# Kernel tuning notes

Measured on AMD Instinct MI355X. Metric: run time of the kernel, lower is better.

Reference implementation:

```python
import jax, jax.numpy as jnp
import numpy as np

N = 50000        # nodes
E = 800000       # edges (avg degree 16)
IN = 256         # in_size
H = 4            # heads
C = 32           # out_size per head
NEG_SLOPE = 0.2  # PyG GATConv leaky_relu slope
LN_EPS = 1e-5


def setup_inputs() -> dict:
    key = jax.random.key(0)
    ks = jax.random.split(key, 6)
    x = jax.random.normal(ks[0], (N, IN), dtype=jnp.float32)
    edge_index = jax.random.randint(ks[1], (2, E), 0, N, dtype=jnp.int32)
    W = jax.random.normal(ks[2], (IN, H * C), dtype=jnp.float32) * 0.05
    att_src = jax.random.normal(ks[3], (H, C), dtype=jnp.float32) * 0.05
    att_dst = jax.random.normal(ks[4], (H, C), dtype=jnp.float32) * 0.05
    bias = jnp.zeros((H * C,), dtype=jnp.float32)
    ln_gamma = jnp.ones((H * C,), dtype=jnp.float32)
    ln_beta = jnp.zeros((H * C,), dtype=jnp.float32)
    return {"x": x, "edge_index": edge_index, "W": W, "att_src": att_src,
            "att_dst": att_dst, "bias": bias, "ln_gamma": ln_gamma,
            "ln_beta": ln_beta}


def _segment_softmax(alpha, seg, num_segments):
    # alpha: [E, H], softmax over edges sharing the same destination node.
    amax = jax.ops.segment_max(alpha, seg, num_segments=num_segments)  # [N, H]
    amax = jnp.where(jnp.isfinite(amax), amax, 0.0)  # nodes with no in-edges
    ex = jnp.exp(alpha - amax[seg])
    denom = jax.ops.segment_sum(ex, seg, num_segments=num_segments)    # [N, H]
    return ex / (denom[seg] + 1e-16)


def reference(x, edge_index, W, att_src, att_dst, bias, ln_gamma, ln_beta):
    # --- GATConv (concat=True) ---
    x_lin = (x @ W).reshape(N, H, C)                    # [N, H, C]
    a_src = jnp.sum(x_lin * att_src, axis=-1)           # [N, H]
    a_dst = jnp.sum(x_lin * att_dst, axis=-1)           # [N, H]
    src, dst = edge_index[0], edge_index[1]             # messages src -> dst
    alpha = a_src[src] + a_dst[dst]                     # [E, H]
    alpha = jnp.where(alpha >= 0, alpha, NEG_SLOPE * alpha)
    alpha = _segment_softmax(alpha, dst, N)             # [E, H]
    msg = x_lin[src] * alpha[..., None]                 # [E, H, C]
    out = jax.ops.segment_sum(msg, dst, num_segments=N) # [N, H, C]
    out = out.reshape(N, H * C) + bias                  # [N, H*C]
    # --- LayerNorm over feature dim ---
    mu = jnp.mean(out, axis=-1, keepdims=True)
    var = jnp.mean(jnp.square(out - mu), axis=-1, keepdims=True)
    out = (out - mu) * jax.lax.rsqrt(var + LN_EPS) * ln_gamma + ln_beta
    # --- activation ---
    return jax.nn.relu(out)
```

## Files before the change

kernel.cpp:

```cpp
#include <hip/hip_runtime.h>

#define NNODES 50000
#define NEDGES 800000
#define INFEAT 256
#define HC 128
#define NH 4
#define CPH 32
#define LSTRIDE 264
#define CSTRIDE 16

typedef unsigned int uint32;
typedef unsigned short u16;
typedef short short8 __attribute__((ext_vector_type(8)));
typedef float f32x4 __attribute__((ext_vector_type(4)));

__device__ __forceinline__ float b2f(u16 s) {
    uint32 u = ((uint32)s) << 16;
    return __builtin_bit_cast(float, u);
}
__device__ __forceinline__ u16 f2bf(float x) {
    uint32 u = __builtin_bit_cast(uint32, x);
    uint32 r = (u + 0x7FFFu + ((u >> 16) & 1u)) >> 16;
    return (u16)r;
}
__device__ __forceinline__ bool probe_bf16(const void* gamma) {
    return ((const uint32*)gamma)[0] == 0x3F803F80u;
}

__global__ __launch_bounds__(256) void wtp_kernel(const void* __restrict__ W,
                                                  const void* __restrict__ gm,
                                                  u16* __restrict__ wtp,
                                                  int* __restrict__ count) {
    const bool isbf = probe_bf16(gm);
    int c = blockIdx.x * 256 + threadIdx.x;
    int kt = c >> 9, nt = (c >> 6) & 7, l = c & 63;
    int r = l & 15, quad = l >> 4;
    int n = nt * 16 + r;
    int kbase = kt * 32 + quad * 8;
    u16 vals[8];
#pragma unroll
    for (int j = 0; j < 8; ++j) {
        int k = kbase + j;
        vals[j] = isbf ? ((const u16*)W)[k * HC + n] : f2bf(((const float*)W)[k * HC + n]);
    }
    *(uint4*)(wtp + (size_t)c * 8) = *(const uint4*)vals;
    uint4 z = {0u, 0u, 0u, 0u};
    uint4* cz = (uint4*)count;
    for (int i = c; i < NNODES * CSTRIDE / 4; i += 4096) cz[i] = z;
}

__global__ __launch_bounds__(256) void hist_kernel(const int* __restrict__ ei,
                                                   int* __restrict__ count,
                                                   int* __restrict__ rank) {
    int eb = blockIdx.x * 1024 + threadIdx.x;
#pragma unroll
    for (int rep = 0; rep < 4; ++rep) {
        int e = eb + rep * 256;
        if (e < NEDGES) rank[e] = atomicAdd(&count[ei[NEDGES + e] * CSTRIDE], 1);
    }
}

__global__ __launch_bounds__(256) void gemm_mfma(const void* __restrict__ x,
                                                 const uint4* __restrict__ wtp,
                                                 const void* __restrict__ att_src,
                                                 const void* __restrict__ att_dst,
                                                 const void* __restrict__ gm,
                                                 u16* __restrict__ xlin,
                                                 float* __restrict__ asrc,
                                                 float* __restrict__ adst) {
    __shared__ u16 atile[4 * 16 * LSTRIDE];
    const bool isbf = probe_bf16(gm);
    const int tid = threadIdx.x;
    const int wv = tid >> 6;
    const int lane = tid & 63;
    int wave = blockIdx.x * 4 + wv;
    int r = lane & 15;
    int quad = lane >> 4;
    int m0 = wave * 16;
    u16* my = atile + wv * (16 * LSTRIDE);

    if (isbf) {
#pragma unroll
        for (int rep = 0; rep < 8; ++rep) {
            int idx = rep * 64 + lane;
            int row = idx >> 5;
            int ch  = idx & 31;
            int gr = m0 + row;
            if (gr > NNODES - 1) gr = NNODES - 1;
            uint4 q = *(const uint4*)((const u16*)x + (size_t)gr * INFEAT + ch * 8);
            *(uint4*)(my + row * LSTRIDE + ch * 8) = q;
        }
    } else {
#pragma unroll
        for (int rep = 0; rep < 16; ++rep) {
            int idx = rep * 64 + lane;
            int row = idx >> 6;
            int c4  = idx & 63;
            int gr = m0 + row;
            if (gr > NNODES - 1) gr = NNODES - 1;
            float4 f = *(const float4*)((const float*)x + (size_t)gr * INFEAT + c4 * 4);
            u16 v[4] = {f2bf(f.x), f2bf(f.y), f2bf(f.z), f2bf(f.w)};
            *(uint2*)(my + row * LSTRIDE + c4 * 4) = *(const uint2*)v;
        }
    }
    __syncthreads();

    f32x4 acc[8];
#pragma unroll
    for (int nt = 0; nt < 8; ++nt) acc[nt] = (f32x4){0.f, 0.f, 0.f, 0.f};

#pragma unroll
    for (int kt = 0; kt < 8; ++kt) {
        short8 afrag = __builtin_bit_cast(short8,
            *(const uint4*)(my + r * LSTRIDE + kt * 32 + quad * 8));
#pragma unroll
        for (int nt = 0; nt < 8; ++nt) {
            short8 bfrag = __builtin_bit_cast(short8, wtp[(kt * 8 + nt) * 64 + lane]);
            acc[nt] = __builtin_amdgcn_mfma_f32_16x16x32_bf16(afrag, bfrag, acc[nt], 0, 0, 0);
        }
    }
#pragma unroll
    for (int nt = 0; nt < 8; ++nt) {
#pragma unroll
        for (int reg = 0; reg < 4; ++reg) {
            int grow = m0 + quad * 4 + reg;
            if (grow < NNODES) xlin[(size_t)grow * HC + nt * 16 + r] = f2bf(acc[nt][reg]);
        }
    }

    float asv[8], adv[8];
#pragma unroll
    for (int nt = 0; nt < 8; ++nt) {
        int c = nt * 16 + r;
        if (isbf) {
            asv[nt] = b2f(((const u16*)att_src)[c]);
            adv[nt] = b2f(((const u16*)att_dst)[c]);
        } else {
            asv[nt] = ((const float*)att_src)[c];
            adv[nt] = ((const float*)att_dst)[c];
        }
    }
    float psrc[4][4], pdst[4][4];
#pragma unroll
    for (int h = 0; h < 4; ++h)
#pragma unroll
        for (int reg = 0; reg < 4; ++reg) { psrc[h][reg] = 0.f; pdst[h][reg] = 0.f; }
#pragma unroll
    for (int nt = 0; nt < 8; ++nt) {
        const int h = nt >> 1;
#pragma unroll
        for (int reg = 0; reg < 4; ++reg) {
            psrc[h][reg] = fmaf(acc[nt][reg], asv[nt], psrc[h][reg]);
            pdst[h][reg] = fmaf(acc[nt][reg], adv[nt], pdst[h][reg]);
        }
    }
#pragma unroll
    for (int m = 1; m < 16; m <<= 1) {
#pragma unroll
        for (int h = 0; h < 4; ++h)
#pragma unroll
            for (int reg = 0; reg < 4; ++reg) {
                psrc[h][reg] += __shfl_xor(psrc[h][reg], m);
                pdst[h][reg] += __shfl_xor(pdst[h][reg], m);
            }
    }
#pragma unroll
    for (int reg = 0; reg < 4; ++reg)
#pragma unroll
        for (int h = 0; h < 4; ++h)
            if (r == reg * 4 + h) {
                int grow = m0 + quad * 4 + reg;
                if (grow < NNODES) {
                    asrc[grow * 4 + h] = psrc[h][reg];
                    adst[grow * 4 + h] = pdst[h][reg];
                }
            }
}

__global__ __launch_bounds__(256) void blkred_kernel(const int* __restrict__ count,
                                                     int* __restrict__ blksum) {
    int i = blockIdx.x * 256 + threadIdx.x;
    int v = (i < NNODES) ? count[i * CSTRIDE] : 0;
#pragma unroll
    for (int m = 1; m < 64; m <<= 1) v += __shfl_xor(v, m);
    __shared__ int s[4];
    if ((threadIdx.x & 63) == 0) s[threadIdx.x >> 6] = v;
    __syncthreads();
    if (threadIdx.x == 0) blksum[blockIdx.x] = s[0] + s[1] + s[2] + s[3];
}

__global__ __launch_bounds__(256) void scanout_kernel(const int* __restrict__ count,
                                                      const int* __restrict__ blksum,
                                                      int* __restrict__ offsets) {
    __shared__ int sb[256];
    __shared__ int sd[256];
    const int nblk = (NNODES + 255) / 256;
    int t = threadIdx.x;
    int bv = (t < nblk) ? blksum[t] : 0;
    sb[t] = bv;
    __syncthreads();
    for (int off = 1; off < 256; off <<= 1) {
        int tv = (t >= off) ? sb[t - off] : 0;
        __syncthreads();
        sb[t] += tv;
        __syncthreads();
    }
    int base = sb[blockIdx.x] - blksum[blockIdx.x];

    int i = blockIdx.x * 256 + t;
    int v = (i < NNODES) ? count[i * CSTRIDE] : 0;
    sd[t] = v;
    __syncthreads();
    for (int off = 1; off < 256; off <<= 1) {
        int tv = (t >= off) ? sd[t - off] : 0;
        __syncthreads();
        sd[t] += tv;
        __syncthreads();
    }
    if (i < NNODES) offsets[i] = base + sd[t] - v;
    if (i == 0) offsets[NNODES] = NEDGES;
}

__global__ __launch_bounds__(256) void scatter_kernel(const int* __restrict__ ei,
                                                      const int* __restrict__ offsets,
                                                      const int* __restrict__ rank,
                                                      int* __restrict__ col) {
    int e = blockIdx.x * 256 + threadIdx.x;
    if (e >= NEDGES) return;
    int d = ei[NEDGES + e];
    col[offsets[d] + rank[e]] = ei[e];
}

__global__ __launch_bounds__(256) void node_kernel(const u16* __restrict__ xlin,
                                                   const float* __restrict__ asrc,
                                                   const float* __restrict__ adst,
                                                   const int* __restrict__ offsets,
                                                   const int* __restrict__ col,
                                                   const void* __restrict__ bias,
                                                   const void* __restrict__ gamma,
                                                   const void* __restrict__ beta,
                                                   void* __restrict__ out) {
    const bool isbf = probe_bf16(gamma);
    int node = blockIdx.x * 4 + (threadIdx.x >> 6);
    int lane = threadIdx.x & 63;
    int h = lane >> 4;
    int f2 = lane * 2;
    float adh = adst[node * 4 + h];
    int start = offsets[node];
    int end = offsets[node + 1];

    float dsum = 0.f, acc0 = 0.f, acc1 = 0.f;
    int i = start;
    for (; i + 7 < end; i += 8) {
        int cc[8];
        uint32 pf[8];
        float aw[8];
#pragma unroll
        for (int j = 0; j < 8; ++j) cc[j] = col[i + j];
#pragma unroll
        for (int j = 0; j < 8; ++j) {
            pf[j] = *(const uint32*)(xlin + (size_t)cc[j] * HC + f2);
            aw[j] = asrc[cc[j] * 4 + h];
        }
#pragma unroll
        for (int j = 0; j < 8; ++j) {
            float a = aw[j] + adh;
            a = (a >= 0.f) ? a : 0.2f * a;
            float w = __expf(a);
            dsum += w;
            float x0 = __builtin_bit_cast(float, pf[j] << 16);
            float x1 = __builtin_bit_cast(float, pf[j] & 0xffff0000u);
            acc0 = fmaf(x0, w, acc0);
            acc1 = fmaf(x1, w, acc1);
        }
    }
    for (; i + 3 < end; i += 4) {
        int cc[4];
        uint32 pf[4];
        float aw[4];
#pragma unroll
        for (int j = 0; j < 4; ++j) cc[j] = col[i + j];
#pragma unroll
        for (int j = 0; j < 4; ++j) {
            pf[j] = *(const uint32*)(xlin + (size_t)cc[j] * HC + f2);
            aw[j] = asrc[cc[j] * 4 + h];
        }
#pragma unroll
        for (int j = 0; j < 4; ++j) {
            float a = aw[j] + adh;
            a = (a >= 0.f) ? a : 0.2f * a;
            float w = __expf(a);
            dsum += w;
            float x0 = __builtin_bit_cast(float, pf[j] << 16);
            float x1 = __builtin_bit_cast(float, pf[j] & 0xffff0000u);
            acc0 = fmaf(x0, w, acc0);
            acc1 = fmaf(x1, w, acc1);
        }
    }
    for (; i < end; ++i) {
        int c = col[i];
        uint32 p = *(const uint32*)(xlin + (size_t)c * HC + f2);
        float a = asrc[c * 4 + h] + adh;
        a = (a >= 0.f) ? a : 0.2f * a;
        float w = __expf(a);
        dsum += w;
        float x0 = __builtin_bit_cast(float, p << 16);
        float x1 = __builtin_bit_cast(float, p & 0xffff0000u);
        acc0 = fmaf(x0, w, acc0);
        acc1 = fmaf(x1, w, acc1);
    }
    float rden = 1.f / (dsum + 1e-16f);

    float bi0, bi1, g0, g1, be0, be1;
    if (isbf) {
        uint32 bb = ((const uint32*)bias)[lane];
        uint32 gg = ((const uint32*)gamma)[lane];
        uint32 eb = ((const uint32*)beta)[lane];
        bi0 = b2f((u16)(bb & 0xffffu)); bi1 = b2f((u16)(bb >> 16));
        g0  = b2f((u16)(gg & 0xffffu)); g1  = b2f((u16)(gg >> 16));
        be0 = b2f((u16)(eb & 0xffffu)); be1 = b2f((u16)(eb >> 16));
    } else {
        float2 tb = ((const float2*)bias)[lane];
        float2 tg = ((const float2*)gamma)[lane];
        float2 te = ((const float2*)beta)[lane];
        bi0 = tb.x; bi1 = tb.y; g0 = tg.x; g1 = tg.y; be0 = te.x; be1 = te.y;
    }
    float v0 = fmaf(acc0, rden, bi0);
    float v1 = fmaf(acc1, rden, bi1);
    float s2 = v0 + v1;
    float q2 = v0 * v0 + v1 * v1;
#pragma unroll
    for (int m = 1; m < 64; m <<= 1) {
        s2 += __shfl_xor(s2, m);
        q2 += __shfl_xor(q2, m);
    }
    float mean = s2 * (1.f / 128.f);
    float var = q2 * (1.f / 128.f) - mean * mean;
    float inv = rsqrtf(var + 1e-5f);
    float d0 = v0 - mean, d1 = v1 - mean;
    float o0 = fmaxf(fmaf(d0 * inv, g0, be0), 0.f);
    float o1 = fmaxf(fmaf(d1 * inv, g1, be1), 0.f);
    if (isbf) {
        uint32 po = (uint32)f2bf(o0) | ((uint32)f2bf(o1) << 16);
        ((uint32*)out)[(size_t)node * 64 + lane] = po;
    } else {
        float2 po; po.x = o0; po.y = o1;
        ((float2*)out)[(size_t)node * 64 + lane] = po;
    }
}

extern "C" void kernel_launch(void* const* d_in, const int* in_sizes, int n_in,
                              void* d_out, int out_size, void* d_ws, size_t ws_size,
                              hipStream_t stream) {
    const void* x       = d_in[0];
    const int*  ei      = (const int*)d_in[1];
    const void* W       = d_in[2];
    const void* att_src = d_in[3];
    const void* att_dst = d_in[4];
    const void* bias    = d_in[5];
    const void* gamma   = d_in[6];
    const void* beta    = d_in[7];

    char* w = (char*)d_ws;
    size_t off = 0;
    u16* xlin    = (u16*)(w + off);   off += 12800000;
    u16* wtp     = (u16*)(w + off);   off += 65536;
    float* asrc  = (float*)(w + off); off += 800000;
    float* adst  = (float*)(w + off); off += 800000;
    int* count   = (int*)(w + off);
    int* col     = (int*)(w + off);   off += 3200000;
    int* offsets = (int*)(w + off);   off += 200016;
    int* rank    = (int*)(w + off);   off += 3200000;
    int* blksum  = (int*)(w + off);   off += 1024;

    const int NBLK = (NNODES + 255) / 256;
    wtp_kernel<<<16, 256, 0, stream>>>(W, gamma, wtp, count);
    hist_kernel<<<(NEDGES + 1023) / 1024, 256, 0, stream>>>(ei, count, rank);
    gemm_mfma<<<(NNODES + 63) / 64, 256, 0, stream>>>(x, (const uint4*)wtp, att_src, att_dst,
                                                      gamma, xlin, asrc, adst);
    blkred_kernel<<<NBLK, 256, 0, stream>>>(count, blksum);
    scanout_kernel<<<NBLK, 256, 0, stream>>>(count, blksum, offsets);
    scatter_kernel<<<(NEDGES + 255) / 256, 256, 0, stream>>>(ei, offsets, rank, col);
    node_kernel<<<NNODES / 4, 256, 0, stream>>>(xlin, asrc, adst, offsets, col,
                                                bias, gamma, beta, d_out);
}
```

Measured before the change: 213.8 us.

## Precompute edge attention weights in CSR order during scatter; densify count array

The scatter kernel now computes the leaky-relu/exp attention weight for all four heads of every edge and writes them in CSR slot order. The node kernel then streams these weights instead of gathering asrc per neighbor and recomputing exp. The count array drops its 16-int padding, and the barrier after the wave-private LDS fill in the GEMM is removed. In exchange it adds a 12.8 MB write and read of per-edge weights, and packs the atomics onto shared cache lines. The new path only runs if the workspace is large enough.

Result: slower. 231.4 us (+8.2%).

```diff
diff --git a/kernel.cpp b/kernel.cpp
--- a/kernel.cpp
+++ b/kernel.cpp
@@ -7,7 +7,6 @@
 #define NH 4
 #define CPH 32
 #define LSTRIDE 264
-#define CSTRIDE 16
 
 typedef unsigned int uint32;
 typedef unsigned short u16;
@@ -46,7 +45,7 @@
     *(uint4*)(wtp + (size_t)c * 8) = *(const uint4*)vals;
     uint4 z = {0u, 0u, 0u, 0u};
     uint4* cz = (uint4*)count;
-    for (int i = c; i < NNODES * CSTRIDE / 4; i += 4096) cz[i] = z;
+    for (int i = c; i < NNODES / 4; i += 4096) cz[i] = z;
 }
 
 __global__ __launch_bounds__(256) void hist_kernel(const int* __restrict__ ei,
@@ -56,7 +55,7 @@
 #pragma unroll
     for (int rep = 0; rep < 4; ++rep) {
         int e = eb + rep * 256;
-        if (e < NEDGES) rank[e] = atomicAdd(&count[ei[NEDGES + e] * CSTRIDE], 1);
+        if (e < NEDGES) rank[e] = atomicAdd(&count[ei[NEDGES + e]], 1);
     }
 }
 
@@ -103,7 +102,6 @@
             *(uint2*)(my + row * LSTRIDE + c4 * 4) = *(const uint2*)v;
         }
     }
-    __syncthreads();
 
     f32x4 acc[8];
 #pragma unroll
@@ -180,7 +178,7 @@
 __global__ __launch_bounds__(256) void blkred_kernel(const int* __restrict__ count,
                                                      int* __restrict__ blksum) {
     int i = blockIdx.x * 256 + threadIdx.x;
-    int v = (i < NNODES) ? count[i * CSTRIDE] : 0;
+    int v = (i < NNODES) ? count[i] : 0;
 #pragma unroll
     for (int m = 1; m < 64; m <<= 1) v += __shfl_xor(v, m);
     __shared__ int s[4];
@@ -208,7 +206,7 @@
     int base = sb[blockIdx.x] - blksum[blockIdx.x];
 
     int i = blockIdx.x * 256 + t;
-    int v = (i < NNODES) ? count[i * CSTRIDE] : 0;
+    int v = (i < NNODES) ? count[i] : 0;
     sd[t] = v;
     __syncthreads();
     for (int off = 1; off < 256; off <<= 1) {
@@ -221,21 +219,39 @@
     if (i == 0) offsets[NNODES] = NEDGES;
 }
 
+template <bool WITHW>
 __global__ __launch_bounds__(256) void scatter_kernel(const int* __restrict__ ei,
                                                       const int* __restrict__ offsets,
                                                       const int* __restrict__ rank,
-                                                      int* __restrict__ col) {
+                                                      const float* __restrict__ asrc,
+                                                      const float* __restrict__ adst,
+                                                      int* __restrict__ col,
+                                                      float* __restrict__ wf) {
     int e = blockIdx.x * 256 + threadIdx.x;
     if (e >= NEDGES) return;
+    int s = ei[e];
     int d = ei[NEDGES + e];
-    col[offsets[d] + rank[e]] = ei[e];
-}
-
+    int slot = offsets[d] + rank[e];
+    col[slot] = s;
+    if (WITHW) {
+        float4 as = *(const float4*)(asrc + (size_t)s * 4);
+        float4 ad = *(const float4*)(adst + (size_t)d * 4);
+        float4 w;
+        float a0 = as.x + ad.x; a0 = (a0 >= 0.f) ? a0 : 0.2f * a0; w.x = __expf(a0);
+        float a1 = as.y + ad.y; a1 = (a1 >= 0.f) ? a1 : 0.2f * a1; w.y = __expf(a1);
+        float a2 = as.z + ad.z; a2 = (a2 >= 0.f) ? a2 : 0.2f * a2; w.z = __expf(a2);
+        float a3 = as.w + ad.w; a3 = (a3 >= 0.f) ? a3 : 0.2f * a3; w.w = __expf(a3);
+        *(float4*)(wf + (size_t)slot * 4) = w;
+    }
+}
+
+template <bool WITHW>
 __global__ __launch_bounds__(256) void node_kernel(const u16* __restrict__ xlin,
                                                    const float* __restrict__ asrc,
                                                    const float* __restrict__ adst,
                                                    const int* __restrict__ offsets,
                                                    const int* __restrict__ col,
+                                                   const float* __restrict__ wf,
                                                    const void* __restrict__ bias,
                                                    const void* __restrict__ gamma,
                                                    const void* __restrict__ beta,
@@ -245,69 +261,124 @@
     int lane = threadIdx.x & 63;
     int h = lane >> 4;
     int f2 = lane * 2;
-    float adh = adst[node * 4 + h];
+    float adh = WITHW ? 0.f : adst[node * 4 + h];
     int start = offsets[node];
     int end = offsets[node + 1];
 
     float dsum = 0.f, acc0 = 0.f, acc1 = 0.f;
     int i = start;
-    for (; i + 7 < end; i += 8) {
-        int cc[8];
-        uint32 pf[8];
-        float aw[8];
-#pragma unroll
-        for (int j = 0; j < 8; ++j) cc[j] = col[i + j];
-#pragma unroll
-        for (int j = 0; j < 8; ++j) {
-            pf[j] = *(const uint32*)(xlin + (size_t)cc[j] * HC + f2);
-            aw[j] = asrc[cc[j] * 4 + h];
-        }
-#pragma unroll
-        for (int j = 0; j < 8; ++j) {
-            float a = aw[j] + adh;
+    if (WITHW) {
+        for (; i + 7 < end; i += 8) {
+            int cc[8];
+            uint32 pf[8];
+            float wv[8];
+#pragma unroll
+            for (int j = 0; j < 8; ++j) cc[j] = col[i + j];
+#pragma unroll
+            for (int j = 0; j < 8; ++j) {
+                pf[j] = *(const uint32*)(xlin + (size_t)cc[j] * HC + f2);
+                wv[j] = wf[(size_t)(i + j) * 4 + h];
+            }
+#pragma unroll
+            for (int j = 0; j < 8; ++j) {
+                float w = wv[j];
+                dsum += w;
+                float x0 = __builtin_bit_cast(float, pf[j] << 16);
+                float x1 = __builtin_bit_cast(float, pf[j] & 0xffff0000u);
+                acc0 = fmaf(x0, w, acc0);
+                acc1 = fmaf(x1, w, acc1);
+            }
+        }
+        for (; i + 3 < end; i += 4) {
+            int cc[4];
+            uint32 pf[4];
+            float wv[4];
+#pragma unroll
+            for (int j = 0; j < 4; ++j) cc[j] = col[i + j];
+#pragma unroll
+            for (int j = 0; j < 4; ++j) {
+                pf[j] = *(const uint32*)(xlin + (size_t)cc[j] * HC + f2);
+                wv[j] = wf[(size_t)(i + j) * 4 + h];
+            }
+#pragma unroll
+            for (int j = 0; j < 4; ++j) {
+                float w = wv[j];
+                dsum += w;
+                float x0 = __builtin_bit_cast(float, pf[j] << 16);
+                float x1 = __builtin_bit_cast(float, pf[j] & 0xffff0000u);
+                acc0 = fmaf(x0, w, acc0);
+                acc1 = fmaf(x1, w, acc1);
+            }
+        }
+        for (; i < end; ++i) {
+            int c = col[i];
+            uint32 p = *(const uint32*)(xlin + (size_t)c * HC + f2);
+            float w = wf[(size_t)i * 4 + h];
+            dsum += w;
+            float x0 = __builtin_bit_cast(float, p << 16);
+            float x1 = __builtin_bit_cast(float, p & 0xffff0000u);
+            acc0 = fmaf(x0, w, acc0);
+            acc1 = fmaf(x1, w, acc1);
+        }
+    } else {
+        for (; i + 7 < end; i += 8) {
+            int cc[8];
+            uint32 pf[8];
+            float aw[8];
+#pragma unroll
+            for (int j = 0; j < 8; ++j) cc[j] = col[i + j];
+#pragma unroll
+            for (int j = 0; j < 8; ++j) {
+                pf[j] = *(const uint32*)(xlin + (size_t)cc[j] * HC + f2);
+                aw[j] = asrc[cc[j] * 4 + h];
+            }
+#pragma unroll
+            for (int j = 0; j < 8; ++j) {
+                float a = aw[j] + adh;
+                a = (a >= 0.f) ? a : 0.2f * a;
+                float w = __expf(a);
+                dsum += w;
+                float x0 = __builtin_bit_cast(float, pf[j] << 16);
+                float x1 = __builtin_bit_cast(float, pf[j] & 0xffff0000u);
+                acc0 = fmaf(x0, w, acc0);
+                acc1 = fmaf(x1, w, acc1);
+            }
+        }
+        for (; i + 3 < end; i += 4) {
+            int cc[4];
+            uint32 pf[4];
+            float aw[4];
+#pragma unroll
+            for (int j = 0; j < 4; ++j) cc[j] = col[i + j];
+#pragma unroll
+            for (int j = 0; j < 4; ++j) {
+                pf[j] = *(const uint32*)(xlin + (size_t)cc[j] * HC + f2);
+                aw[j] = asrc[cc[j] * 4 + h];
+            }
+#pragma unroll
+            for (int j = 0; j < 4; ++j) {
+                float a = aw[j] + adh;
+                a = (a >= 0.f) ? a : 0.2f * a;
+                float w = __expf(a);
+                dsum += w;
+                float x0 = __builtin_bit_cast(float, pf[j] << 16);
+                float x1 = __builtin_bit_cast(float, pf[j] & 0xffff0000u);
+                acc0 = fmaf(x0, w, acc0);
+                acc1 = fmaf(x1, w, acc1);
+            }
+        }
+        for (; i < end; ++i) {
+            int c = col[i];
+            uint32 p = *(const uint32*)(xlin + (size_t)c * HC + f2);
+            float a = asrc[c * 4 + h] + adh;
             a = (a >= 0.f) ? a : 0.2f * a;
             float w = __expf(a);
             dsum += w;
-            float x0 = __builtin_bit_cast(float, pf[j] << 16);
-            float x1 = __builtin_bit_cast(float, pf[j] & 0xffff0000u);
+            float x0 = __builtin_bit_cast(float, p << 16);
+            float x1 = __builtin_bit_cast(float, p & 0xffff0000u);
             acc0 = fmaf(x0, w, acc0);
             acc1 = fmaf(x1, w, acc1);
         }
-    }
-    for (; i + 3 < end; i += 4) {
-        int cc[4];
-        uint32 pf[4];
-        float aw[4];
-#pragma unroll
-        for (int j = 0; j < 4; ++j) cc[j] = col[i + j];
-#pragma unroll
-        for (int j = 0; j < 4; ++j) {
-            pf[j] = *(const uint32*)(xlin + (size_t)cc[j] * HC + f2);
-            aw[j] = asrc[cc[j] * 4 + h];
-        }
-#pragma unroll
-        for (int j = 0; j < 4; ++j) {
-            float a = aw[j] + adh;
-            a = (a >= 0.f) ? a : 0.2f * a;
-            float w = __expf(a);
-            dsum += w;
-            float x0 = __builtin_bit_cast(float, pf[j] << 16);
-            float x1 = __builtin_bit_cast(float, pf[j] & 0xffff0000u);
-            acc0 = fmaf(x0, w, acc0);
-            acc1 = fmaf(x1, w, acc1);
-        }
-    }
-    for (; i < end; ++i) {
-        int c = col[i];
-        uint32 p = *(const uint32*)(xlin + (size_t)c * HC + f2);
-        float a = asrc[c * 4 + h] + adh;
-        a = (a >= 0.f) ? a : 0.2f * a;
-        float w = __expf(a);
-        dsum += w;
-        float x0 = __builtin_bit_cast(float, p << 16);
-        float x1 = __builtin_bit_cast(float, p & 0xffff0000u);
-        acc0 = fmaf(x0, w, acc0);
-        acc1 = fmaf(x1, w, acc1);
     }
     float rden = 1.f / (dsum + 1e-16f);
 
@@ -367,11 +438,14 @@
     u16* wtp     = (u16*)(w + off);   off += 65536;
     float* asrc  = (float*)(w + off); off += 800000;
     float* adst  = (float*)(w + off); off += 800000;
-    int* count   = (int*)(w + off);
-    int* col     = (int*)(w + off);   off += 3200000;
+    int* count   = (int*)(w + off);   off += 200000;
     int* offsets = (int*)(w + off);   off += 200016;
     int* rank    = (int*)(w + off);   off += 3200000;
     int* blksum  = (int*)(w + off);   off += 1024;
+    int* col     = (int*)(w + off);   off += 3200000;
+    float* wf    = (float*)(w + off); off += 12800000;
+
+    const bool withw = (ws_size >= off);
 
     const int NBLK = (NNODES + 255) / 256;
     wtp_kernel<<<16, 256, 0, stream>>>(W, gamma, wtp, count);
@@ -380,7 +454,15 @@
                                                       gamma, xlin, asrc, adst);
     blkred_kernel<<<NBLK, 256, 0, stream>>>(count, blksum);
     scanout_kernel<<<NBLK, 256, 0, stream>>>(count, blksum, offsets);
-    scatter_kernel<<<(NEDGES + 255) / 256, 256, 0, stream>>>(ei, offsets, rank, col);
-    node_kernel<<<NNODES / 4, 256, 0, stream>>>(xlin, asrc, adst, offsets, col,
-                                                bias, gamma, beta, d_out);
-}
+    if (withw) {
+        scatter_kernel<true><<<(NEDGES + 255) / 256, 256, 0, stream>>>(ei, offsets, rank,
+                                                                       asrc, adst, col, wf);
+        node_kernel<true><<<NNODES / 4, 256, 0, stream>>>(xlin, asrc, adst, offsets, col, wf,
+                                                          bias, gamma, beta, d_out);
+    } else {
+        scatter_kernel<false><<<(NEDGES + 255) / 256, 256, 0, stream>>>(ei, offsets, rank,
+                                                                        asrc, adst, col, wf);
+        node_kernel<false><<<NNODES / 4, 256, 0, stream>>>(xlin, asrc, adst, offsets, col, wf,
+                                                           bias, gamma, beta, d_out);
+    }
+}
```

## Compute edge attention weights once per edge in LDS, compact count array

Applied to the files above, without the earlier changes.

The node aggregation kernel now has one lane per edge in a 64-edge chunk. That lane loads the source index and all four head logits, computes the leaky-relu exponentials once, and stages the weights and indices in per-wave LDS. The gather-and-accumulate loop then reads them from LDS, which removes the redundant per-lane exp and asrc gathers the old code did for every lane sharing a head. The in-degree count array is also unpadded so hist, blkred and scan read it densely, which may raise atomic contention within a cache line. A block barrier in the GEMM is dropped because each wave only reads its own LDS tile.

Measured after the change: 212.7 us. No clear change (-0.5%).

```diff
diff --git a/kernel.cpp b/kernel.cpp
--- a/kernel.cpp
+++ b/kernel.cpp
@@ -7,7 +7,7 @@
 #define NH 4
 #define CPH 32
 #define LSTRIDE 264
-#define CSTRIDE 16
+#define WSTR 68
 
 typedef unsigned int uint32;
 typedef unsigned short u16;
@@ -25,6 +25,9 @@
 }
 __device__ __forceinline__ bool probe_bf16(const void* gamma) {
     return ((const uint32*)gamma)[0] == 0x3F803F80u;
+}
+__device__ __forceinline__ float expleaky(float a) {
+    return __expf(fmaxf(a, 0.2f * a));
 }
 
 __global__ __launch_bounds__(256) void wtp_kernel(const void* __restrict__ W,
@@ -46,7 +49,7 @@
     *(uint4*)(wtp + (size_t)c * 8) = *(const uint4*)vals;
     uint4 z = {0u, 0u, 0u, 0u};
     uint4* cz = (uint4*)count;
-    for (int i = c; i < NNODES * CSTRIDE / 4; i += 4096) cz[i] = z;
+    for (int i = c; i < NNODES / 4; i += 4096) cz[i] = z;
 }
 
 __global__ __launch_bounds__(256) void hist_kernel(const int* __restrict__ ei,
@@ -56,7 +59,7 @@
 #pragma unroll
     for (int rep = 0; rep < 4; ++rep) {
         int e = eb + rep * 256;
-        if (e < NEDGES) rank[e] = atomicAdd(&count[ei[NEDGES + e] * CSTRIDE], 1);
+        if (e < NEDGES) rank[e] = atomicAdd(&count[ei[NEDGES + e]], 1);
     }
 }
 
@@ -103,7 +106,6 @@
             *(uint2*)(my + row * LSTRIDE + c4 * 4) = *(const uint2*)v;
         }
     }
-    __syncthreads();
 
     f32x4 acc[8];
 #pragma unroll
@@ -180,7 +182,7 @@
 __global__ __launch_bounds__(256) void blkred_kernel(const int* __restrict__ count,
                                                      int* __restrict__ blksum) {
     int i = blockIdx.x * 256 + threadIdx.x;
-    int v = (i < NNODES) ? count[i * CSTRIDE] : 0;
+    int v = (i < NNODES) ? count[i] : 0;
 #pragma unroll
     for (int m = 1; m < 64; m <<= 1) v += __shfl_xor(v, m);
     __shared__ int s[4];
@@ -208,7 +210,7 @@
     int base = sb[blockIdx.x] - blksum[blockIdx.x];
 
     int i = blockIdx.x * 256 + t;
-    int v = (i < NNODES) ? count[i * CSTRIDE] : 0;
+    int v = (i < NNODES) ? count[i] : 0;
     sd[t] = v;
     __syncthreads();
     for (int off = 1; off < 256; off <<= 1) {
@@ -240,74 +242,97 @@
                                                    const void* __restrict__ gamma,
                                                    const void* __restrict__ beta,
                                                    void* __restrict__ out) {
+    __shared__ float wlds[4][4 * WSTR];
+    __shared__ int   slds[4][64];
     const bool isbf = probe_bf16(gamma);
-    int node = blockIdx.x * 4 + (threadIdx.x >> 6);
-    int lane = threadIdx.x & 63;
+    const int wv = threadIdx.x >> 6;
+    const int lane = threadIdx.x & 63;
+    int node = blockIdx.x * 4 + wv;
     int h = lane >> 4;
     int f2 = lane * 2;
-    float adh = adst[node * 4 + h];
     int start = offsets[node];
     int end = offsets[node + 1];
+    float4 ad4 = *(const float4*)(adst + (size_t)node * 4);
 
     float dsum = 0.f, acc0 = 0.f, acc1 = 0.f;
-    int i = start;
-    for (; i + 7 < end; i += 8) {
-        int cc[8];
-        uint32 pf[8];
-        float aw[8];
-#pragma unroll
-        for (int j = 0; j < 8; ++j) cc[j] = col[i + j];
-#pragma unroll
-        for (int j = 0; j < 8; ++j) {
-            pf[j] = *(const uint32*)(xlin + (size_t)cc[j] * HC + f2);
-            aw[j] = asrc[cc[j] * 4 + h];
-        }
-#pragma unroll
-        for (int j = 0; j < 8; ++j) {
-            float a = aw[j] + adh;
-            a = (a >= 0.f) ? a : 0.2f * a;
-            float w = __expf(a);
+    float* wmy = wlds[wv];
+    int* smy = slds[wv];
+
+    for (int base = start; base < end; base += 64) {
+        int cnt = end - base;
+        if (cnt > 64) cnt = 64;
+        float4 w4 = {0.f, 0.f, 0.f, 0.f};
+        int src = 0;
+        if (lane < cnt) {
+            src = col[base + lane];
+            float4 as4 = *(const float4*)(asrc + (size_t)src * 4);
+            w4.x = expleaky(as4.x + ad4.x);
+            w4.y = expleaky(as4.y + ad4.y);
+            w4.z = expleaky(as4.z + ad4.z);
+            w4.w = expleaky(as4.w + ad4.w);
+        }
+        smy[lane] = src;
+        wmy[0 * WSTR + lane] = w4.x;
+        wmy[1 * WSTR + lane] = w4.y;
+        wmy[2 * WSTR + lane] = w4.z;
+        wmy[3 * WSTR + lane] = w4.w;
+
+        const float* wh = wmy + h * WSTR;
+        int j = 0;
+        for (; j + 7 < cnt; j += 8) {
+            float4 wa = *(const float4*)(wh + j);
+            float4 wb = *(const float4*)(wh + j + 4);
+            int4 sa = *(const int4*)(smy + j);
+            int4 sb = *(const int4*)(smy + j + 4);
+            uint32 pf[8];
+            pf[0] = *(const uint32*)(xlin + (size_t)sa.x * HC + f2);
+            pf[1] = *(const uint32*)(xlin + (size_t)sa.y * HC + f2);
+            pf[2] = *(const uint32*)(xlin + (size_t)sa.z * HC + f2);
+            pf[3] = *(const uint32*)(xlin + (size_t)sa.w * HC + f2);
+            pf[4] = *(const uint32*)(xlin + (size_t)sb.x * HC + f2);
+            pf[5] = *(const uint32*)(xlin + (size_t)sb.y * HC + f2);
+            pf[6] = *(const uint32*)(xlin + (size_t)sb.z * HC + f2);
+            pf[7] = *(const uint32*)(xlin + (size_t)sb.w * HC + f2);
+            float wv8[8] = {wa.x, wa.y, wa.z, wa.w, wb.x, wb.y, wb.z, wb.w};
+#pragma unroll
+            for (int k = 0; k < 8; ++k) {
+                float w = wv8[k];
+                dsum += w;
+                float x0 = __builtin_bit_cast(float, pf[k] << 16);
+                float x1 = __builtin_bit_cast(float, pf[k] & 0xffff0000u);
+                acc0 = fmaf(x0, w, acc0);
+                acc1 = fmaf(x1, w, acc1);
+            }
+        }
+        for (; j + 3 < cnt; j += 4) {
+            float4 wa = *(const float4*)(wh + j);
+            int4 sa = *(const int4*)(smy + j);
+            uint32 pf[4];
+            pf[0] = *(const uint32*)(xlin + (size_t)sa.x * HC + f2);
+            pf[1] = *(const uint32*)(xlin + (size_t)sa.y * HC + f2);
+            pf[2] = *(const uint32*)(xlin + (size_t)sa.z * HC + f2);
+            pf[3] = *(const uint32*)(xlin + (size_t)sa.w * HC + f2);
+            float wv4[4] = {wa.x, wa.y, wa.z, wa.w};
+#pragma unroll
+            for (int k = 0; k < 4; ++k) {
+                float w = wv4[k];
+                dsum += w;
+                float x0 = __builtin_bit_cast(float, pf[k] << 16);
+                float x1 = __builtin_bit_cast(float, pf[k] & 0xffff0000u);
+                acc0 = fmaf(x0, w, acc0);
+                acc1 = fmaf(x1, w, acc1);
+            }
+        }
+        for (; j < cnt; ++j) {
+            float w = wh[j];
+            int c = smy[j];
+            uint32 p = *(const uint32*)(xlin + (size_t)c * HC + f2);
             dsum += w;
-            float x0 = __builtin_bit_cast(float, pf[j] << 16);
-            float x1 = __builtin_bit_cast(float, pf[j] & 0xffff0000u);
+            float x0 = __builtin_bit_cast(float, p << 16);
+            float x1 = __builtin_bit_cast(float, p & 0xffff0000u);
             acc0 = fmaf(x0, w, acc0);
             acc1 = fmaf(x1, w, acc1);
         }
-    }
-    for (; i + 3 < end; i += 4) {
-        int cc[4];
-        uint32 pf[4];
-        float aw[4];
-#pragma unroll
-        for (int j = 0; j < 4; ++j) cc[j] = col[i + j];
-#pragma unroll
-        for (int j = 0; j < 4; ++j) {
-            pf[j] = *(const uint32*)(xlin + (size_t)cc[j] * HC + f2);
-            aw[j] = asrc[cc[j] * 4 + h];
-        }
-#pragma unroll
-        for (int j = 0; j < 4; ++j) {
-            float a = aw[j] + adh;
-            a = (a >= 0.f) ? a : 0.2f * a;
-            float w = __expf(a);
-            dsum += w;
-            float x0 = __builtin_bit_cast(float, pf[j] << 16);
-            float x1 = __builtin_bit_cast(float, pf[j] & 0xffff0000u);
-            acc0 = fmaf(x0, w, acc0);
-            acc1 = fmaf(x1, w, acc1);
-        }
-    }
-    for (; i < end; ++i) {
-        int c = col[i];
-        uint32 p = *(const uint32*)(xlin + (size_t)c * HC + f2);
-        float a = asrc[c * 4 + h] + adh;
-        a = (a >= 0.f) ? a : 0.2f * a;
-        float w = __expf(a);
-        dsum += w;
-        float x0 = __builtin_bit_cast(float, p << 16);
-        float x1 = __builtin_bit_cast(float, p & 0xffff0000u);
-        acc0 = fmaf(x0, w, acc0);
-        acc1 = fmaf(x1, w, acc1);
     }
     float rden = 1.f / (dsum + 1e-16f);
 
@@ -367,11 +392,11 @@
     u16* wtp     = (u16*)(w + off);   off += 65536;
     float* asrc  = (float*)(w + off); off += 800000;
     float* adst  = (float*)(w + off); off += 800000;
-    int* count   = (int*)(w + off);
-    int* col     = (int*)(w + off);   off += 3200000;
+    int* count   = (int*)(w + off);   off += 200000;
     int* offsets = (int*)(w + off);   off += 200016;
     int* rank    = (int*)(w + off);   off += 3200000;
     int* blksum  = (int*)(w + off);   off += 1024;
+    int* col     = (int*)(w + off);   off += 3200000;
 
     const int NBLK = (NNODES + 255) / 256;
     wtp_kernel<<<16, 256, 0, stream>>>(W, gamma, wtp, count);
```
